# Optimization experiments

Measured on AMD Instinct MI355X. Metric: run time of the kernel, lower is better.

The kernel has to match this reference:

```python
import jax, jax.numpy as jnp
import numpy as np


def setup_inputs() -> dict:
    key = jax.random.key(0)
    k1, k2, k3 = jax.random.split(key, 3)
    bs, nvars, T, input_dim = 8, 16, 512, 256
    embed_dim, num_embed, codebook_num = 128, 512, 4
    inp = jax.random.normal(k1, (bs, nvars, T, input_dim), dtype=jnp.float32)
    # xavier_normal_ for (input_dim, embed_dim): std = sqrt(2/(fan_in+fan_out))
    xavier_std = float(np.sqrt(2.0 / (input_dim + embed_dim)))
    projector = jax.random.normal(k2, (input_dim, embed_dim), dtype=jnp.float32) * xavier_std
    codebook = jax.random.normal(k3, (codebook_num, num_embed, embed_dim), dtype=jnp.float32)
    return {"input": inp, "projector": projector, "codebook": codebook}


def reference(input, projector, codebook):
    # project: [b,n,t,input_dim] @ [input_dim,embed_dim] -> [b,n,t,d]
    x = jnp.matmul(input, projector)
    # L2-normalize along last dim (matches torch .norm(dim=-1,keepdim=True) division)
    x = x / jnp.linalg.norm(x, axis=-1, keepdims=True)
    cb = codebook / jnp.linalg.norm(codebook, axis=-1, keepdims=True)
    # cosine similarity: [b,n,t,c,m]
    similarity = jnp.einsum('bntd,cmd->bntcm', x, cb)
    # nearest code per codebook: [b,n,t,c]
    idx = jnp.argmax(similarity, axis=-1)
    return idx
```

## Files before the change

### kernel.cpp

```cpp
#include <hip/hip_runtime.h>
#include <math.h>

#define DIN    256
#define DEMB   128
#define NCB    4
#define MCODES 512
#define NCODE  2048
#define MARGIN 1.5e-4f

using bf16x8 = __attribute__((ext_vector_type(8))) short;
using f32x16 = __attribute__((ext_vector_type(16))) float;

static __device__ __forceinline__ unsigned short f2bf(float f) {
    unsigned u = __float_as_uint(f);
    u += 0x7FFFu + ((u >> 16) & 1u);
    return (unsigned short)(u >> 16);
}
static __device__ __forceinline__ float bf2f(unsigned short h) {
    return __uint_as_float(((unsigned)h) << 16);
}
static __device__ __forceinline__ float4 ld4(const float* p) {
    return *reinterpret_cast<const float4*>(p);
}
static __device__ __forceinline__ unsigned umaxu(unsigned a, unsigned b) { return a > b ? a : b; }
static __device__ __forceinline__ unsigned uminu(unsigned a, unsigned b) { return a < b ? a : b; }
static __device__ __forceinline__ void gload_lds16(const void* g, void* l) {
    __builtin_amdgcn_global_load_lds(
        (const __attribute__((address_space(1))) void*)g,
        (__attribute__((address_space(3))) void*)l, 16, 0, 0);
}

__global__ __launch_bounds__(256) void prep_codebook(
        const float* __restrict__ cb, float* __restrict__ cbn,
        unsigned short* __restrict__ cbA) {
    const int w = threadIdx.x >> 6, lane = threadIdx.x & 63;
    const int code = blockIdx.x * 4 + w;
    const float2 v = reinterpret_cast<const float2*>(cb + (size_t)code * DEMB)[lane];
    float ss = v.x * v.x + v.y * v.y;
#pragma unroll
    for (int m = 1; m < 64; m <<= 1) ss += __shfl_xor(ss, m, 64);
    const float rn = 1.0f / sqrtf(ss);
    const float x0 = v.x * rn, x1 = v.y * rn;
    reinterpret_cast<float2*>(cbn + (size_t)code * DEMB)[lane] = make_float2(x0, x1);

    const unsigned short h0 = f2bf(x0), h1 = f2bf(x1);
    const unsigned short l0 = f2bf(x0 - bf2f(h0)), l1 = f2bf(x1 - bf2f(h1));
    const int ct = code >> 5, ci = code & 31;
    const int kt = lane >> 3, g = (lane >> 2) & 1, i = 2 * (lane & 3);
    const size_t base = ((size_t)ct * 1024 + kt * 128 + g * 32 + ci) * 8 + i;
    *reinterpret_cast<ushort2*>(cbA + base)       = make_ushort2(h0, h1);
    *reinterpret_cast<ushort2*>(cbA + base + 512) = make_ushort2(l0, l1);
}

__global__ __launch_bounds__(256) void prep_proj(
        const float* __restrict__ proj, unsigned short* __restrict__ pjA) {
    const int t = blockIdx.x * 256 + threadIdx.x;
    const int ci = t & 31, g = (t >> 5) & 1, kt = (t >> 6) & 15, mt = t >> 10;
    const int m = mt * 32 + ci;
    const size_t base = ((size_t)(mt * 16 + kt) * 3) * 512 + (size_t)(g * 32 + ci) * 8;
#pragma unroll
    for (int i = 0; i < 8; ++i) {
        const float v = proj[(size_t)(kt * 16 + g * 8 + i) * DEMB + m];
        const unsigned short h = f2bf(v);
        const float r1 = v - bf2f(h);
        const unsigned short md = f2bf(r1);
        const float r2 = r1 - bf2f(md);
        pjA[base + i]        = h;
        pjA[base + 512 + i]  = md;
        pjA[base + 1024 + i] = f2bf(r2);
    }
}

__global__ __launch_bounds__(256) void project_mfma(
        const float* __restrict__ inp, const unsigned short* __restrict__ pjA,
        float* __restrict__ xw) {
    const int tid = threadIdx.x;
    const int lane = tid & 63, mt = tid >> 6, kg = lane >> 5;
    const int row = blockIdx.x * 32 + (lane & 31);
    const float* xr = inp + (size_t)row * DIN;
    const unsigned short* pL = pjA + (size_t)lane * 8;

    auto ldin = [&](float4& a, float4& b, int kt) {
        a = ld4(xr + kt * 16 + kg * 8);
        b = ld4(xr + kt * 16 + kg * 8 + 4);
    };
    auto ldA = [&](bf16x8& h, bf16x8& m, bf16x8& l, int kt) {
        const unsigned short* pf = pL + ((size_t)(mt * 16 + kt) * 3) * 512;
        h = *reinterpret_cast<const bf16x8*>(pf);
        m = *reinterpret_cast<const bf16x8*>(pf + 512);
        l = *reinterpret_cast<const bf16x8*>(pf + 1024);
    };

    f32x16 P, Q;
#pragma unroll
    for (int r = 0; r < 16; ++r) { P[r] = 0.0f; Q[r] = 0.0f; }

    auto do_step = [&](const float4& c0, const float4& c1,
                       const bf16x8& Ah, const bf16x8& Am, const bf16x8& Al) {
        const float xs[8] = {c0.x, c0.y, c0.z, c0.w, c1.x, c1.y, c1.z, c1.w};
        bf16x8 Bh, Bm, Bl;
#pragma unroll
        for (int e = 0; e < 8; ++e) {
            const float v = xs[e];
            const unsigned short h = f2bf(v);
            const float r1 = v - bf2f(h);
            const unsigned short md = f2bf(r1);
            const float r2 = r1 - bf2f(md);
            Bh[e] = (short)h; Bm[e] = (short)md; Bl[e] = (short)f2bf(r2);
        }
        P = __builtin_amdgcn_mfma_f32_32x32x16_bf16(Ah, Bh, P, 0, 0, 0);
        Q = __builtin_amdgcn_mfma_f32_32x32x16_bf16(Ah, Bm, Q, 0, 0, 0);
        Q = __builtin_amdgcn_mfma_f32_32x32x16_bf16(Am, Bh, Q, 0, 0, 0);
        Q = __builtin_amdgcn_mfma_f32_32x32x16_bf16(Ah, Bl, Q, 0, 0, 0);
        Q = __builtin_amdgcn_mfma_f32_32x32x16_bf16(Al, Bh, Q, 0, 0, 0);
        Q = __builtin_amdgcn_mfma_f32_32x32x16_bf16(Am, Bm, Q, 0, 0, 0);
    };

    float4 iA0, iA1, iB0, iB1;
    bf16x8 hA, mA, lA, hB, mB, lB;
    ldin(iA0, iA1, 0); ldA(hA, mA, lA, 0);
    ldin(iB0, iB1, 1); ldA(hB, mB, lB, 1);

#pragma unroll 1
    for (int kt = 0; kt < 16; kt += 2) {
        do_step(iA0, iA1, hA, mA, lA);
        if (kt + 2 < 16) { ldin(iA0, iA1, kt + 2); ldA(hA, mA, lA, kt + 2); }
        do_step(iB0, iB1, hB, mB, lB);
        if (kt + 3 < 16) { ldin(iB0, iB1, kt + 3); ldA(hB, mB, lB, kt + 3); }
    }

#pragma unroll
    for (int q = 0; q < 4; ++q) {
        float4 v;
        v.x = P[q * 4 + 0] + Q[q * 4 + 0];
        v.y = P[q * 4 + 1] + Q[q * 4 + 1];
        v.z = P[q * 4 + 2] + Q[q * 4 + 2];
        v.w = P[q * 4 + 3] + Q[q * 4 + 3];
        *reinterpret_cast<float4*>(xw + (size_t)row * DEMB + mt * 32 + q * 8 + kg * 4) = v;
    }
}

__global__ __launch_bounds__(256) void project_kernel(
        const float* __restrict__ inp, const float* __restrict__ proj,
        float* __restrict__ xw) {
    const int tid = threadIdx.x, tx = tid & 31, ty = tid >> 5;
    const int rowBase = blockIdx.x * 64;

    float acc1[8][4];
#pragma unroll
    for (int i = 0; i < 8; ++i)
#pragma unroll
        for (int j = 0; j < 4; ++j) acc1[i][j] = 0.0f;

    const float* inRow0 = inp + (size_t)(rowBase + ty) * DIN;
    const float* pjCol  = proj + tx * 4;

    float4 ivA[8], ivB[8], pjA[4], pjB[4];
    auto load_step = [&](float4 iv[8], float4 pj[4], int kk) {
#pragma unroll
        for (int j = 0; j < 4; ++j) pj[j] = ld4(pjCol + (size_t)(kk + j) * DEMB);
#pragma unroll
        for (int i = 0; i < 8; ++i) iv[i] = ld4(inRow0 + (size_t)(8 * i) * DIN + kk);
    };
    auto fma_step = [&](const float4 iv[8], const float4 pj[4]) {
#pragma unroll
        for (int i = 0; i < 8; ++i) {
            const float* ivp = reinterpret_cast<const float*>(&iv[i]);
#pragma unroll
            for (int j = 0; j < 4; ++j) {
                acc1[i][0] = fmaf(ivp[j], pj[j].x, acc1[i][0]);
                acc1[i][1] = fmaf(ivp[j], pj[j].y, acc1[i][1]);
                acc1[i][2] = fmaf(ivp[j], pj[j].z, acc1[i][2]);
                acc1[i][3] = fmaf(ivp[j], pj[j].w, acc1[i][3]);
            }
        }
    };
    load_step(ivA, pjA, 0);
#pragma unroll 1
    for (int k = 0; k < DIN; k += 8) {
        load_step(ivB, pjB, k + 4);
        fma_step(ivA, pjA);
        if (k + 8 < DIN) load_step(ivA, pjA, k + 8);
        fma_step(ivB, pjB);
    }
#pragma unroll
    for (int i = 0; i < 8; ++i) {
        const int r = rowBase + ty + 8 * i;
        *reinterpret_cast<float4*>(xw + (size_t)r * DEMB + tx * 4) =
            make_float4(acc1[i][0], acc1[i][1], acc1[i][2], acc1[i][3]);
    }
}

__global__ __launch_bounds__(256) void sim_kernel(
        const float* __restrict__ xw,
        const unsigned short* __restrict__ cbA,
        int* __restrict__ out, int* __restrict__ unc_cnt,
        int* __restrict__ unc_list) {
    __shared__ __align__(16) short sA[3][8192];
    const int tid = threadIdx.x;
    const int lane = tid & 63, wv = tid >> 6;
    const int kg = lane >> 5;
    const int cbi = blockIdx.x & 3;
    const int rowBase = (blockIdx.x >> 2) * 128;
    const int row = rowBase + wv * 32 + (lane & 31);

    const short* gA = (const short*)cbA + (size_t)cbi * 16 * 8192;
    auto stage = [&](int buf, int t) {
        const short* g = gA + (size_t)t * 8192 + wv * 2048 + lane * 8;
        short* l = &sA[buf][wv * 2048];
#pragma unroll
        for (int c = 0; c < 4; ++c)
            gload_lds16(g + c * 512, l + c * 512);
    };

    stage(0, 0);
    stage(1, 1);

    bf16x8 Bhi[8], Blo[8];
    {
        const float* xr = xw + (size_t)row * DEMB;
        float4 f0[8], f1[8];
        float ss = 0.0f;
#pragma unroll
        for (int kt = 0; kt < 8; ++kt) {
            f0[kt] = ld4(xr + kt * 16 + kg * 8);
            f1[kt] = ld4(xr + kt * 16 + kg * 8 + 4);
            ss += f0[kt].x * f0[kt].x + f0[kt].y * f0[kt].y +
                  f0[kt].z * f0[kt].z + f0[kt].w * f0[kt].w +
                  f1[kt].x * f1[kt].x + f1[kt].y * f1[kt].y +
                  f1[kt].z * f1[kt].z + f1[kt].w * f1[kt].w;
        }
        ss += __shfl_xor(ss, 32, 64);
        const float rn = 1.0f / sqrtf(ss);
#pragma unroll
        for (int kt = 0; kt < 8; ++kt) {
            const float xs[8] = {f0[kt].x, f0[kt].y, f0[kt].z, f0[kt].w,
                                 f1[kt].x, f1[kt].y, f1[kt].z, f1[kt].w};
            bf16x8 hv, lv;
#pragma unroll
            for (int e = 0; e < 8; ++e) {
                const float xn = xs[e] * rn;
                const unsigned short h = f2bf(xn);
                hv[e] = (short)h;
                lv[e] = (short)f2bf(xn - bf2f(h));
            }
            Bhi[kt] = hv; Blo[kt] = lv;
        }
    }

    f32x16 TWO;
#pragma unroll
    for (int r = 0; r < 16; ++r) TWO[r] = 2.0f;

    f32x16 acc = TWO;
    unsigned t1k = 0u, t2k = 0u; int btile = 0;

    auto epi = [&](const f32x16& pAcc, int gprev) {
        const unsigned prev = t1k;
#pragma unroll
        for (int r = 0; r < 16; ++r) {
            const unsigned kb = (__float_as_uint(pAcc[r]) & 0xFFFFFFF0u) | (15u - (unsigned)r);
            t2k = umaxu(t2k, uminu(kb, t1k));
            t1k = umaxu(t1k, kb);
        }
        if (t1k != prev) btile = gprev;
    };

#pragma unroll 1
    for (int g = 0; g < 16; ++g) {
        if (g < 15) asm volatile("s_waitcnt vmcnt(4)" ::: "memory");
        else        asm volatile("s_waitcnt vmcnt(0)" ::: "memory");
        __builtin_amdgcn_s_barrier();
        asm volatile("" ::: "memory");
        if (g + 2 < 16) stage((g + 2) % 3, g + 2);

        const short* pa = &sA[g % 3][lane * 8];
        const f32x16 pAcc = acc;
#pragma unroll
        for (int kt = 0; kt < 8; ++kt) {
            const bf16x8 Ahi = *reinterpret_cast<const bf16x8*>(pa + kt * 1024);
            const bf16x8 Alo = *reinterpret_cast<const bf16x8*>(pa + kt * 1024 + 512);
            acc = __builtin_amdgcn_mfma_f32_32x32x16_bf16(Ahi, Bhi[kt], kt ? acc : TWO, 0, 0, 0);
            acc = __builtin_amdgcn_mfma_f32_32x32x16_bf16(Ahi, Blo[kt], acc, 0, 0, 0);
            acc = __builtin_amdgcn_mfma_f32_32x32x16_bf16(Alo, Bhi[kt], acc, 0, 0, 0);
        }

        if (g > 0) epi(pAcc, g - 1);
    }
    epi(acc, 15);

    const unsigned o1 = (unsigned)__shfl_xor((int)t1k, 32, 64);
    const unsigned o2 = (unsigned)__shfl_xor((int)t2k, 32, 64);
    const int     obt = __shfl_xor(btile, 32, 64);
    const unsigned m2k = umaxu(umaxu(t2k, o2), uminu(t1k, o1));
    const unsigned w1k = umaxu(t1k, o1);
    const int wkg = (o1 > t1k) ? (kg ^ 1) : kg;
    const int wbt = (o1 > t1k) ? obt : btile;
    const float gap = __uint_as_float(w1k & 0xFFFFFFF0u) -
                      __uint_as_float(m2k & 0xFFFFFFF0u);
    const bool unc = gap < MARGIN;
    const int rr = 15 - (int)(w1k & 0xFu);
    const int code = wbt * 32 + (rr & 3) + 8 * (rr >> 2) + 4 * wkg;
    if (lane < 32 && !unc)
        out[(size_t)row * NCB + cbi] = code;

    unsigned long long msk = __ballot(unc && lane < 32);
    if (lane == 0 && msk) {
        const int n = __popcll(msk);
        int base = atomicAdd(unc_cnt, n);
        while (msk) {
            const int r = __ffsll(msk) - 1; msk &= msk - 1;
            unc_list[base++] = ((rowBase + wv * 32 + r) << 2) | cbi;
        }
    }
}

__global__ __launch_bounds__(256) void recheck_kernel(
        const float* __restrict__ inp, const float* __restrict__ proj,
        const float* __restrict__ cbn,
        const int* __restrict__ unc_cnt, const int* __restrict__ unc_list,
        int* __restrict__ out) {
    __shared__ float sx[DEMB];
    __shared__ float sBest[4];
    __shared__ int   sIdx[4];
    const int lane = threadIdx.x & 63, wv = threadIdx.x >> 6;
    const int n = *unc_cnt;
    for (int it = blockIdx.x; it < n; it += gridDim.x) {
        const int item = unc_list[it];
        const int row = item >> 2, cbi = item & 3;
        if (wv == 0) {
            const float* ir = inp + (size_t)row * DIN;
            float a0 = 0.0f, a1 = 0.0f;
#pragma unroll 2
            for (int k = 0; k < DIN; k += 4) {
                const float4 iv = ld4(ir + k);
                const float* ivp = reinterpret_cast<const float*>(&iv);
#pragma unroll
                for (int j = 0; j < 4; ++j) {
                    a0 = fmaf(ivp[j], proj[(size_t)(k + j) * DEMB + lane],      a0);
                    a1 = fmaf(ivp[j], proj[(size_t)(k + j) * DEMB + lane + 64], a1);
                }
            }
            sx[lane] = a0; sx[lane + 64] = a1;
        }
        __syncthreads();

        float best = -INFINITY; int bi = 0;
#pragma unroll
        for (int j = 0; j < 2; ++j) {
            const int c = wv * 128 + lane + 64 * j;
            const float* cv = cbn + ((size_t)cbi * MCODES + c) * DEMB;
            float s0 = 0, s1 = 0, s2 = 0, s3 = 0;
#pragma unroll 4
            for (int k = 0; k < DEMB; k += 4) {
                const float4 xk = ld4(&sx[k]);
                const float4 ck = ld4(cv + k);
                s0 = fmaf(xk.x, ck.x, s0); s1 = fmaf(xk.y, ck.y, s1);
                s2 = fmaf(xk.z, ck.z, s2); s3 = fmaf(xk.w, ck.w, s3);
            }
            const float s = (s0 + s1) + (s2 + s3);
            if (s > best) { best = s; bi = c; }
        }
#pragma unroll
        for (int mm = 1; mm < 64; mm <<= 1) {
            const float ov = __shfl_xor(best, mm, 64);
            const int   oc = __shfl_xor(bi, mm, 64);
            if (ov > best || (ov == best && oc < bi)) { best = ov; bi = oc; }
        }
        if (lane == 0) { sBest[wv] = best; sIdx[wv] = bi; }
        __syncthreads();
        if (wv == 0 && lane == 0) {
            float b = sBest[0]; int bidx = sIdx[0];
#pragma unroll
            for (int w = 1; w < 4; ++w) {
                if (sBest[w] > b) { b = sBest[w]; bidx = sIdx[w]; }
            }
            out[(size_t)row * NCB + cbi] = bidx;
        }
        __syncthreads();
    }
}

__global__ __launch_bounds__(256) void fused_quantize_kernel(
        const float* __restrict__ inp, const float* __restrict__ proj,
        const float* __restrict__ cbn, const unsigned short* __restrict__ cbA,
        int* __restrict__ out) {
    __shared__ float sX[128][132];
    __shared__ float sRn[128];
    const int tid = threadIdx.x;
    const int tx = tid & 31, ty = tid >> 5;
    const int rowBase = blockIdx.x * 128;

#pragma unroll 1
    for (int p = 0; p < 2; ++p) {
        float acc1[8][4];
#pragma unroll
        for (int i = 0; i < 8; ++i)
#pragma unroll
            for (int j = 0; j < 4; ++j) acc1[i][j] = 0.0f;
        const float* inRow0 = inp + (size_t)(rowBase + p * 64 + ty) * DIN;
        const float* pjCol  = proj + tx * 4;
        float4 ivA[8], ivB[8], pjA[4], pjB[4];
        auto load_step = [&](float4 iv[8], float4 pj[4], int kk) {
#pragma unroll
            for (int j = 0; j < 4; ++j) pj[j] = ld4(pjCol + (size_t)(kk + j) * DEMB);
#pragma unroll
            for (int i = 0; i < 8; ++i) iv[i] = ld4(inRow0 + (size_t)(8 * i) * DIN + kk);
        };
        auto fma_step = [&](const float4 iv[8], const float4 pj[4]) {
#pragma unroll
            for (int i = 0; i < 8; ++i) {
                const float* ivp = reinterpret_cast<const float*>(&iv[i]);
#pragma unroll
                for (int j = 0; j < 4; ++j) {
                    acc1[i][0] = fmaf(ivp[j], pj[j].x, acc1[i][0]);
                    acc1[i][1] = fmaf(ivp[j], pj[j].y, acc1[i][1]);
                    acc1[i][2] = fmaf(ivp[j], pj[j].z, acc1[i][2]);
                    acc1[i][3] = fmaf(ivp[j], pj[j].w, acc1[i][3]);
                }
            }
        };
        load_step(ivA, pjA, 0);
#pragma unroll 1
        for (int k = 0; k < DIN; k += 8) {
            load_step(ivB, pjB, k + 4);
            fma_step(ivA, pjA);
            if (k + 8 < DIN) load_step(ivA, pjA, k + 8);
            fma_step(ivB, pjB);
        }
#pragma unroll
        for (int i = 0; i < 8; ++i) {
            const int r = p * 64 + ty + 8 * i;
            float ss = acc1[i][0] * acc1[i][0] + acc1[i][1] * acc1[i][1] +
                       acc1[i][2] * acc1[i][2] + acc1[i][3] * acc1[i][3];
#pragma unroll
            for (int mm = 1; mm < 32; mm <<= 1) ss += __shfl_xor(ss, mm, 64);
            if (tx == 0) sRn[r] = 1.0f / sqrtf(ss);
            *reinterpret_cast<float4*>(&sX[r][tx * 4]) =
                make_float4(acc1[i][0], acc1[i][1], acc1[i][2], acc1[i][3]);
        }
    }
    __syncthreads();

    const int lane = tid & 63, wv = tid >> 6;
    const int kg = lane >> 5;
    const int rowL = wv * 32 + (lane & 31);
    bf16x8 Bhi[8], Blo[8];
    {
        const float rn = sRn[rowL];
#pragma unroll
        for (int kt = 0; kt < 8; ++kt) {
            const int k0 = kt * 16 + kg * 8;
            float4 f0 = ld4(&sX[rowL][k0]);
            float4 f1 = ld4(&sX[rowL][k0 + 4]);
            float xs[8] = {f0.x, f0.y, f0.z, f0.w, f1.x, f1.y, f1.z, f1.w};
            bf16x8 hv, lv;
#pragma unroll
            for (int e = 0; e < 8; ++e) {
                const float xn = xs[e] * rn;
                const unsigned short h = f2bf(xn);
                hv[e] = (short)h;
                lv[e] = (short)f2bf(xn - bf2f(h));
            }
            Bhi[kt] = hv; Blo[kt] = lv;
        }
    }
    float t1 = -INFINITY, t2 = -INFINITY; int i1 = 0;
    const short* pA = reinterpret_cast<const short*>(cbA) + (size_t)lane * 8;
#pragma unroll 1
    for (int ct = 0; ct < 64; ++ct) {
        if ((ct & 1) == 0) __syncthreads();
        const short* pct = pA + (size_t)ct * 8192;
        f32x16 accA, accB;
#pragma unroll
        for (int r = 0; r < 16; ++r) { accA[r] = 0.0f; accB[r] = 0.0f; }
#pragma unroll
        for (int kt = 0; kt < 8; ++kt) {
            const bf16x8 Ahi = *reinterpret_cast<const bf16x8*>(pct + kt * 1024);
            const bf16x8 Alo = *reinterpret_cast<const bf16x8*>(pct + kt * 1024 + 512);
            accA = __builtin_amdgcn_mfma_f32_32x32x16_bf16(Ahi, Bhi[kt], accA, 0, 0, 0);
            accB = __builtin_amdgcn_mfma_f32_32x32x16_bf16(Ahi, Blo[kt], accB, 0, 0, 0);
            accB = __builtin_amdgcn_mfma_f32_32x32x16_bf16(Alo, Bhi[kt], accB, 0, 0, 0);
        }
#pragma unroll
        for (int r = 0; r < 16; ++r) {
            const float v = accA[r] + accB[r];
            const int gidx = ct * 32 + ((r & 3) + 8 * (r >> 2) + 4 * kg);
            t2 = fmaxf(t2, fminf(v, t1));
            if (v > t1) { t1 = v; i1 = gidx; }
        }
        if ((ct & 15) == 15) {
            const int cbi = ct >> 4;
            const float o1 = __shfl_xor(t1, 32, 64);
            const float o2 = __shfl_xor(t2, 32, 64);
            const int   oi = __shfl_xor(i1, 32, 64);
            const float m2 = fmaxf(fmaxf(t2, o2), fminf(t1, o1));
            if (o1 > t1 || (o1 == t1 && oi < i1)) { t1 = o1; i1 = oi; }
            const bool unc = (t1 - m2) < MARGIN;
            if (lane < 32 && !unc)
                out[(size_t)(rowBase + rowL) * NCB + cbi] = i1 - cbi * MCODES;
            unsigned long long msk = __ballot(unc && lane < 32);
            while (msk) {
                const int r = __ffsll(msk) - 1; msk &= msk - 1;
                const int rl = wv * 32 + r;
                float best = -INFINITY; int bi = 0;
#pragma unroll 1
                for (int j = 0; j < 8; ++j) {
                    const int c = lane + 64 * j;
                    const float* cv = cbn + ((size_t)cbi * MCODES + c) * DEMB;
                    float s0 = 0, s1 = 0, s2 = 0, s3 = 0;
#pragma unroll
                    for (int k = 0; k < DEMB; k += 4) {
                        const float4 xk = ld4(&sX[rl][k]);
                        const float4 ck = ld4(cv + k);
                        s0 = fmaf(xk.x, ck.x, s0); s1 = fmaf(xk.y, ck.y, s1);
                        s2 = fmaf(xk.z, ck.z, s2); s3 = fmaf(xk.w, ck.w, s3);
                    }
                    const float s = (s0 + s1) + (s2 + s3);
                    if (s > best) { best = s; bi = c; }
                }
#pragma unroll
                for (int mm = 1; mm < 64; mm <<= 1) {
                    const float ov = __shfl_xor(best, mm, 64);
                    const int   oc = __shfl_xor(bi, mm, 64);
                    if (ov > best || (ov == best && oc < bi)) { best = ov; bi = oc; }
                }
                if (lane == 0) out[(size_t)(rowBase + rl) * NCB + cbi] = bi;
            }
            t1 = -INFINITY; t2 = -INFINITY; i1 = 0;
        }
    }
}

extern "C" void kernel_launch(void* const* d_in, const int* in_sizes, int n_in,
                              void* d_out, int out_size, void* d_ws, size_t ws_size,
                              hipStream_t stream) {
    const float* inp  = (const float*)d_in[0];
    const float* proj = (const float*)d_in[1];
    const float* cb   = (const float*)d_in[2];
    int* out = (int*)d_out;

    char* ws = (char*)d_ws;
    float* cbn = (float*)ws;
    unsigned short* cbA = (unsigned short*)(ws + (1 << 20));
    float* xw  = (float*)(ws + (2 << 20) + (1 << 18));
    const size_t off_cnt = (size_t)(2 << 20) + (1 << 18) + ((size_t)32 << 20);
    int* unc_cnt  = (int*)(ws + off_cnt);
    int* unc_list = (int*)(ws + off_cnt + 256);
    const size_t off_pjA = off_cnt + 256 + (1 << 20);
    unsigned short* pjA = (unsigned short*)(ws + off_pjA);
    const size_t need_old = off_pjA;
    const size_t need_new = off_pjA + 192 * 1024;

    hipLaunchKernelGGL(prep_codebook, dim3(NCODE / 4), dim3(256), 0, stream,
                       cb, cbn, cbA);
    if (ws_size >= need_old) {
        hipMemsetAsync(unc_cnt, 0, 4, stream);
        if (ws_size >= need_new) {
            hipLaunchKernelGGL(prep_proj, dim3(16), dim3(256), 0, stream, proj, pjA);
            hipLaunchKernelGGL(project_mfma, dim3(2048), dim3(256), 0, stream,
                               inp, pjA, xw);
        } else {
            hipLaunchKernelGGL(project_kernel, dim3(1024), dim3(256), 0, stream,
                               inp, proj, xw);
        }
        hipLaunchKernelGGL(sim_kernel, dim3(2048), dim3(256), 0, stream,
                           xw, cbA, out, unc_cnt, unc_list);
        hipLaunchKernelGGL(recheck_kernel, dim3(2048), dim3(256), 0, stream,
                           inp, proj, cbn, unc_cnt, unc_list, out);
    } else {
        hipLaunchKernelGGL(fused_quantize_kernel, dim3(512), dim3(256), 0, stream,
                           inp, proj, cbn, cbA, out);
    }
}
```

Measured before the change: 211.1 us.

## Fuse MFMA projection into similarity kernel and loop over all codebooks per block

Merges the projection GEMM into the similarity kernel, so each 128-row block computes its projected rows in registers, normalizes them through cross-half shuffles, and then streams all four codebooks (64 tiles) instead of one. This removes the 32 MB xw intermediate write and read, one kernel launch, and the four-fold repeat of the x load and normalization per codebook. In exchange the grid shrinks from 2048 to 512 blocks, register pressure rises with eight accumulator tiles, and the fallback project_kernel path is dropped.

```diff
diff --git a/kernel.cpp b/kernel.cpp
--- a/kernel.cpp
+++ b/kernel.cpp
@@ -71,32 +71,41 @@
     }
 }
 
-__global__ __launch_bounds__(256) void project_mfma(
+__global__ __launch_bounds__(256) void sim_fused_kernel(
         const float* __restrict__ inp, const unsigned short* __restrict__ pjA,
-        float* __restrict__ xw) {
+        const unsigned short* __restrict__ cbA,
+        int* __restrict__ out, int* __restrict__ unc_cnt,
+        int* __restrict__ unc_list) {
+    __shared__ __align__(16) short sA[3][8192];
     const int tid = threadIdx.x;
-    const int lane = tid & 63, mt = tid >> 6, kg = lane >> 5;
-    const int row = blockIdx.x * 32 + (lane & 31);
+    const int lane = tid & 63, wv = tid >> 6;
+    const int kg = lane >> 5;
+    const int rowBase = blockIdx.x * 128;
+    const int row = rowBase + wv * 32 + (lane & 31);
+
+    auto stage = [&](int buf, int t) {
+        const short* g = (const short*)cbA + (size_t)t * 8192 + wv * 2048 + lane * 8;
+        short* l = &sA[buf][wv * 2048];
+#pragma unroll
+        for (int c = 0; c < 4; ++c)
+            gload_lds16(g + c * 512, l + c * 512);
+    };
+    stage(0, 0);
+    stage(1, 1);
+
     const float* xr = inp + (size_t)row * DIN;
     const unsigned short* pL = pjA + (size_t)lane * 8;
+    f32x16 accP[4], accQ[4];
+#pragma unroll
+    for (int mt = 0; mt < 4; ++mt)
+#pragma unroll
+        for (int r = 0; r < 16; ++r) { accP[mt][r] = 0.0f; accQ[mt][r] = 0.0f; }
 
     auto ldin = [&](float4& a, float4& b, int kt) {
         a = ld4(xr + kt * 16 + kg * 8);
         b = ld4(xr + kt * 16 + kg * 8 + 4);
     };
-    auto ldA = [&](bf16x8& h, bf16x8& m, bf16x8& l, int kt) {
-        const unsigned short* pf = pL + ((size_t)(mt * 16 + kt) * 3) * 512;
-        h = *reinterpret_cast<const bf16x8*>(pf);
-        m = *reinterpret_cast<const bf16x8*>(pf + 512);
-        l = *reinterpret_cast<const bf16x8*>(pf + 1024);
-    };
-
-    f32x16 P, Q;
-#pragma unroll
-    for (int r = 0; r < 16; ++r) { P[r] = 0.0f; Q[r] = 0.0f; }
-
-    auto do_step = [&](const float4& c0, const float4& c1,
-                       const bf16x8& Ah, const bf16x8& Am, const bf16x8& Al) {
+    auto do_step = [&](const float4& c0, const float4& c1, int kt) {
         const float xs[8] = {c0.x, c0.y, c0.z, c0.w, c1.x, c1.y, c1.z, c1.w};
         bf16x8 Bh, Bm, Bl;
 #pragma unroll
@@ -108,144 +117,70 @@
             const float r2 = r1 - bf2f(md);
             Bh[e] = (short)h; Bm[e] = (short)md; Bl[e] = (short)f2bf(r2);
         }
-        P = __builtin_amdgcn_mfma_f32_32x32x16_bf16(Ah, Bh, P, 0, 0, 0);
-        Q = __builtin_amdgcn_mfma_f32_32x32x16_bf16(Ah, Bm, Q, 0, 0, 0);
-        Q = __builtin_amdgcn_mfma_f32_32x32x16_bf16(Am, Bh, Q, 0, 0, 0);
-        Q = __builtin_amdgcn_mfma_f32_32x32x16_bf16(Ah, Bl, Q, 0, 0, 0);
-        Q = __builtin_amdgcn_mfma_f32_32x32x16_bf16(Al, Bh, Q, 0, 0, 0);
-        Q = __builtin_amdgcn_mfma_f32_32x32x16_bf16(Am, Bm, Q, 0, 0, 0);
+#pragma unroll
+        for (int mt = 0; mt < 4; ++mt) {
+            const unsigned short* pf = pL + ((size_t)(mt * 16 + kt) * 3) * 512;
+            const bf16x8 Ah = *reinterpret_cast<const bf16x8*>(pf);
+            const bf16x8 Am = *reinterpret_cast<const bf16x8*>(pf + 512);
+            const bf16x8 Al = *reinterpret_cast<const bf16x8*>(pf + 1024);
+            accP[mt] = __builtin_amdgcn_mfma_f32_32x32x16_bf16(Ah, Bh, accP[mt], 0, 0, 0);
+            accQ[mt] = __builtin_amdgcn_mfma_f32_32x32x16_bf16(Ah, Bm, accQ[mt], 0, 0, 0);
+            accQ[mt] = __builtin_amdgcn_mfma_f32_32x32x16_bf16(Am, Bh, accQ[mt], 0, 0, 0);
+            accQ[mt] = __builtin_amdgcn_mfma_f32_32x32x16_bf16(Ah, Bl, accQ[mt], 0, 0, 0);
+            accQ[mt] = __builtin_amdgcn_mfma_f32_32x32x16_bf16(Al, Bh, accQ[mt], 0, 0, 0);
+            accQ[mt] = __builtin_amdgcn_mfma_f32_32x32x16_bf16(Am, Bm, accQ[mt], 0, 0, 0);
+        }
     };
 
     float4 iA0, iA1, iB0, iB1;
-    bf16x8 hA, mA, lA, hB, mB, lB;
-    ldin(iA0, iA1, 0); ldA(hA, mA, lA, 0);
-    ldin(iB0, iB1, 1); ldA(hB, mB, lB, 1);
-
+    ldin(iA0, iA1, 0);
+    ldin(iB0, iB1, 1);
 #pragma unroll 1
     for (int kt = 0; kt < 16; kt += 2) {
-        do_step(iA0, iA1, hA, mA, lA);
-        if (kt + 2 < 16) { ldin(iA0, iA1, kt + 2); ldA(hA, mA, lA, kt + 2); }
-        do_step(iB0, iB1, hB, mB, lB);
-        if (kt + 3 < 16) { ldin(iB0, iB1, kt + 3); ldA(hB, mB, lB, kt + 3); }
-    }
-
-#pragma unroll
-    for (int q = 0; q < 4; ++q) {
-        float4 v;
-        v.x = P[q * 4 + 0] + Q[q * 4 + 0];
-        v.y = P[q * 4 + 1] + Q[q * 4 + 1];
-        v.z = P[q * 4 + 2] + Q[q * 4 + 2];
-        v.w = P[q * 4 + 3] + Q[q * 4 + 3];
-        *reinterpret_cast<float4*>(xw + (size_t)row * DEMB + mt * 32 + q * 8 + kg * 4) = v;
-    }
-}
-
-__global__ __launch_bounds__(256) void project_kernel(
-        const float* __restrict__ inp, const float* __restrict__ proj,
-        float* __restrict__ xw) {
-    const int tid = threadIdx.x, tx = tid & 31, ty = tid >> 5;
-    const int rowBase = blockIdx.x * 64;
-
-    float acc1[8][4];
-#pragma unroll
-    for (int i = 0; i < 8; ++i)
-#pragma unroll
-        for (int j = 0; j < 4; ++j) acc1[i][j] = 0.0f;
-
-    const float* inRow0 = inp + (size_t)(rowBase + ty) * DIN;
-    const float* pjCol  = proj + tx * 4;
-
-    float4 ivA[8], ivB[8], pjA[4], pjB[4];
-    auto load_step = [&](float4 iv[8], float4 pj[4], int kk) {
-#pragma unroll
-        for (int j = 0; j < 4; ++j) pj[j] = ld4(pjCol + (size_t)(kk + j) * DEMB);
-#pragma unroll
-        for (int i = 0; i < 8; ++i) iv[i] = ld4(inRow0 + (size_t)(8 * i) * DIN + kk);
-    };
-    auto fma_step = [&](const float4 iv[8], const float4 pj[4]) {
-#pragma unroll
-        for (int i = 0; i < 8; ++i) {
-            const float* ivp = reinterpret_cast<const float*>(&iv[i]);
-#pragma unroll
-            for (int j = 0; j < 4; ++j) {
-                acc1[i][0] = fmaf(ivp[j], pj[j].x, acc1[i][0]);
-                acc1[i][1] = fmaf(ivp[j], pj[j].y, acc1[i][1]);
-                acc1[i][2] = fmaf(ivp[j], pj[j].z, acc1[i][2]);
-                acc1[i][3] = fmaf(ivp[j], pj[j].w, acc1[i][3]);
-            }
-        }
-    };
-    load_step(ivA, pjA, 0);
-#pragma unroll 1
-    for (int k = 0; k < DIN; k += 8) {
-        load_step(ivB, pjB, k + 4);
-        fma_step(ivA, pjA);
-        if (k + 8 < DIN) load_step(ivA, pjA, k + 8);
-        fma_step(ivB, pjB);
-    }
-#pragma unroll
-    for (int i = 0; i < 8; ++i) {
-        const int r = rowBase + ty + 8 * i;
-        *reinterpret_cast<float4*>(xw + (size_t)r * DEMB + tx * 4) =
-            make_float4(acc1[i][0], acc1[i][1], acc1[i][2], acc1[i][3]);
-    }
-}
-
-__global__ __launch_bounds__(256) void sim_kernel(
-        const float* __restrict__ xw,
-        const unsigned short* __restrict__ cbA,
-        int* __restrict__ out, int* __restrict__ unc_cnt,
-        int* __restrict__ unc_list) {
-    __shared__ __align__(16) short sA[3][8192];
-    const int tid = threadIdx.x;
-    const int lane = tid & 63, wv = tid >> 6;
-    const int kg = lane >> 5;
-    const int cbi = blockIdx.x & 3;
-    const int rowBase = (blockIdx.x >> 2) * 128;
-    const int row = rowBase + wv * 32 + (lane & 31);
-
-    const short* gA = (const short*)cbA + (size_t)cbi * 16 * 8192;
-    auto stage = [&](int buf, int t) {
-        const short* g = gA + (size_t)t * 8192 + wv * 2048 + lane * 8;
-        short* l = &sA[buf][wv * 2048];
-#pragma unroll
-        for (int c = 0; c < 4; ++c)
-            gload_lds16(g + c * 512, l + c * 512);
-    };
-
-    stage(0, 0);
-    stage(1, 1);
+        do_step(iA0, iA1, kt);
+        if (kt + 2 < 16) ldin(iA0, iA1, kt + 2);
+        do_step(iB0, iB1, kt + 1);
+        if (kt + 3 < 16) ldin(iB0, iB1, kt + 3);
+    }
+
+#pragma unroll
+    for (int mt = 0; mt < 4; ++mt)
+#pragma unroll
+        for (int r = 0; r < 16; ++r) accP[mt][r] += accQ[mt][r];
+
+    float ss = 0.0f;
+#pragma unroll
+    for (int mt = 0; mt < 4; ++mt)
+#pragma unroll
+        for (int r = 0; r < 16; ++r) ss += accP[mt][r] * accP[mt][r];
+    ss += __shfl_xor(ss, 32, 64);
+    const float rn = 1.0f / sqrtf(ss);
 
     bf16x8 Bhi[8], Blo[8];
-    {
-        const float* xr = xw + (size_t)row * DEMB;
-        float4 f0[8], f1[8];
-        float ss = 0.0f;
-#pragma unroll
-        for (int kt = 0; kt < 8; ++kt) {
-            f0[kt] = ld4(xr + kt * 16 + kg * 8);
-            f1[kt] = ld4(xr + kt * 16 + kg * 8 + 4);
-            ss += f0[kt].x * f0[kt].x + f0[kt].y * f0[kt].y +
-                  f0[kt].z * f0[kt].z + f0[kt].w * f0[kt].w +
-                  f1[kt].x * f1[kt].x + f1[kt].y * f1[kt].y +
-                  f1[kt].z * f1[kt].z + f1[kt].w * f1[kt].w;
-        }
-        ss += __shfl_xor(ss, 32, 64);
-        const float rn = 1.0f / sqrtf(ss);
-#pragma unroll
-        for (int kt = 0; kt < 8; ++kt) {
-            const float xs[8] = {f0[kt].x, f0[kt].y, f0[kt].z, f0[kt].w,
-                                 f1[kt].x, f1[kt].y, f1[kt].z, f1[kt].w};
-            bf16x8 hv, lv;
-#pragma unroll
-            for (int e = 0; e < 8; ++e) {
-                const float xn = xs[e] * rn;
-                const unsigned short h = f2bf(xn);
-                hv[e] = (short)h;
-                lv[e] = (short)f2bf(xn - bf2f(h));
-            }
-            Bhi[kt] = hv; Blo[kt] = lv;
-        }
+#pragma unroll
+    for (int kt2 = 0; kt2 < 8; ++kt2) {
+        const int mt = kt2 >> 1;
+        float fv[8];
+#pragma unroll
+        for (int j = 0; j < 4; ++j) {
+            const int rLo = j + 8 * (kt2 & 1);
+            const float a = accP[mt][rLo];
+            const float b = accP[mt][rLo + 4];
+            const float own  = kg ? b : a;
+            const float give = kg ? a : b;
+            const float got  = __shfl_xor(give, 32, 64);
+            fv[j]     = kg ? got : own;
+            fv[4 + j] = kg ? own : got;
+        }
+        bf16x8 hv, lv;
+#pragma unroll
+        for (int e = 0; e < 8; ++e) {
+            const float xn = fv[e] * rn;
+            const unsigned short h = f2bf(xn);
+            hv[e] = (short)h;
+            lv[e] = (short)f2bf(xn - bf2f(h));
+        }
+        Bhi[kt2] = hv; Blo[kt2] = lv;
     }
 
     f32x16 TWO;
@@ -255,7 +190,7 @@
     f32x16 acc = TWO;
     unsigned t1k = 0u, t2k = 0u; int btile = 0;
 
-    auto epi = [&](const f32x16& pAcc, int gprev) {
+    auto epi = [&](const f32x16& pAcc, int tileInCb) {
         const unsigned prev = t1k;
 #pragma unroll
         for (int r = 0; r < 16; ++r) {
@@ -263,16 +198,42 @@
             t2k = umaxu(t2k, uminu(kb, t1k));
             t1k = umaxu(t1k, kb);
         }
-        if (t1k != prev) btile = gprev;
+        if (t1k != prev) btile = tileInCb;
     };
+    auto finalize = [&](int cb) {
+        const unsigned o1 = (unsigned)__shfl_xor((int)t1k, 32, 64);
+        const unsigned o2 = (unsigned)__shfl_xor((int)t2k, 32, 64);
+        const int     obt = __shfl_xor(btile, 32, 64);
+        const unsigned m2k = umaxu(umaxu(t2k, o2), uminu(t1k, o1));
+        const unsigned w1k = umaxu(t1k, o1);
+        const int wkg = (o1 > t1k) ? (kg ^ 1) : kg;
+        const int wbt = (o1 > t1k) ? obt : btile;
+        const float gap = __uint_as_float(w1k & 0xFFFFFFF0u) -
+                          __uint_as_float(m2k & 0xFFFFFFF0u);
+        const bool unc = gap < MARGIN;
+        const int rr = 15 - (int)(w1k & 0xFu);
+        const int code = wbt * 32 + (rr & 3) + 8 * (rr >> 2) + 4 * wkg;
+        if (lane < 32 && !unc)
+            out[(size_t)row * NCB + cb] = code;
+        unsigned long long msk = __ballot(unc && lane < 32);
+        if (lane == 0 && msk) {
+            const int n = __popcll(msk);
+            int base = atomicAdd(unc_cnt, n);
+            while (msk) {
+                const int r = __ffsll(msk) - 1; msk &= msk - 1;
+                unc_list[base++] = ((rowBase + wv * 32 + r) << 2) | cb;
+            }
+        }
+        t1k = 0u; t2k = 0u; btile = 0;
+    };
 
 #pragma unroll 1
-    for (int g = 0; g < 16; ++g) {
-        if (g < 15) asm volatile("s_waitcnt vmcnt(4)" ::: "memory");
+    for (int g = 0; g < 64; ++g) {
+        if (g < 63) asm volatile("s_waitcnt vmcnt(4)" ::: "memory");
         else        asm volatile("s_waitcnt vmcnt(0)" ::: "memory");
         __builtin_amdgcn_s_barrier();
         asm volatile("" ::: "memory");
-        if (g + 2 < 16) stage((g + 2) % 3, g + 2);
+        if (g + 2 < 64) stage((g + 2) % 3, g + 2);
 
         const short* pa = &sA[g % 3][lane * 8];
         const f32x16 pAcc = acc;
@@ -285,34 +246,13 @@
             acc = __builtin_amdgcn_mfma_f32_32x32x16_bf16(Alo, Bhi[kt], acc, 0, 0, 0);
         }
 
-        if (g > 0) epi(pAcc, g - 1);
+        if (g > 0) {
+            epi(pAcc, (g - 1) & 15);
+            if ((g & 15) == 0) finalize((g >> 4) - 1);
+        }
     }
     epi(acc, 15);
-
-    const unsigned o1 = (unsigned)__shfl_xor((int)t1k, 32, 64);
-    const unsigned o2 = (unsigned)__shfl_xor((int)t2k, 32, 64);
-    const int     obt = __shfl_xor(btile, 32, 64);
-    const unsigned m2k = umaxu(umaxu(t2k, o2), uminu(t1k, o1));
-    const unsigned w1k = umaxu(t1k, o1);
-    const int wkg = (o1 > t1k) ? (kg ^ 1) : kg;
-    const int wbt = (o1 > t1k) ? obt : btile;
-    const float gap = __uint_as_float(w1k & 0xFFFFFFF0u) -
-                      __uint_as_float(m2k & 0xFFFFFFF0u);
-    const bool unc = gap < MARGIN;
-    const int rr = 15 - (int)(w1k & 0xFu);
-    const int code = wbt * 32 + (rr & 3) + 8 * (rr >> 2) + 4 * wkg;
-    if (lane < 32 && !unc)
-        out[(size_t)row * NCB + cbi] = code;
-
-    unsigned long long msk = __ballot(unc && lane < 32);
-    if (lane == 0 && msk) {
-        const int n = __popcll(msk);
-        int base = atomicAdd(unc_cnt, n);
-        while (msk) {
-            const int r = __ffsll(msk) - 1; msk &= msk - 1;
-            unc_list[base++] = ((rowBase + wv * 32 + r) << 2) | cbi;
-        }
-    }
+    finalize(3);
 }
 
 __global__ __launch_bounds__(256) void recheck_kernel(
@@ -543,29 +483,18 @@
     char* ws = (char*)d_ws;
     float* cbn = (float*)ws;
     unsigned short* cbA = (unsigned short*)(ws + (1 << 20));
-    float* xw  = (float*)(ws + (2 << 20) + (1 << 18));
-    const size_t off_cnt = (size_t)(2 << 20) + (1 << 18) + ((size_t)32 << 20);
-    int* unc_cnt  = (int*)(ws + off_cnt);
-    int* unc_list = (int*)(ws + off_cnt + 256);
-    const size_t off_pjA = off_cnt + 256 + (1 << 20);
-    unsigned short* pjA = (unsigned short*)(ws + off_pjA);
-    const size_t need_old = off_pjA;
-    const size_t need_new = off_pjA + 192 * 1024;
+    int* unc_cnt  = (int*)(ws + (2 << 20));
+    int* unc_list = (int*)(ws + (2 << 20) + 256);
+    unsigned short* pjA = (unsigned short*)(ws + (3 << 20) + 256);
+    const size_t need = ((size_t)3 << 20) + 256 + 192 * 1024;
 
     hipLaunchKernelGGL(prep_codebook, dim3(NCODE / 4), dim3(256), 0, stream,
                        cb, cbn, cbA);
-    if (ws_size >= need_old) {
+    if (ws_size >= need) {
         hipMemsetAsync(unc_cnt, 0, 4, stream);
-        if (ws_size >= need_new) {
-            hipLaunchKernelGGL(prep_proj, dim3(16), dim3(256), 0, stream, proj, pjA);
-            hipLaunchKernelGGL(project_mfma, dim3(2048), dim3(256), 0, stream,
-                               inp, pjA, xw);
-        } else {
-            hipLaunchKernelGGL(project_kernel, dim3(1024), dim3(256), 0, stream,
-                               inp, proj, xw);
-        }
-        hipLaunchKernelGGL(sim_kernel, dim3(2048), dim3(256), 0, stream,
-                           xw, cbA, out, unc_cnt, unc_list);
+        hipLaunchKernelGGL(prep_proj, dim3(16), dim3(256), 0, stream, proj, pjA);
+        hipLaunchKernelGGL(sim_fused_kernel, dim3(512), dim3(256), 0, stream,
+                           inp, pjA, cbA, out, unc_cnt, unc_list);
         hipLaunchKernelGGL(recheck_kernel, dim3(2048), dim3(256), 0, stream,
                            inp, proj, cbn, unc_cnt, unc_list, out);
     } else {
```

After: 231.1 us. +9.5%, slower.
